# Performance work log

Hardware: AMD Instinct MI355X
Metric: run time of the kernel (lower is better)

## Reference

```python
import jax, jax.numpy as jnp
import numpy as np

B = 131072
E = 116            # embedding dim; 12 + E = 128 = layer_sizes[0]
H = 256            # MLP hidden
LATENT = 64

PAIRS = [(0, 1), (0, 2), (1, 2)]
IDS = np.array([[0, 3, 4], [1, 5, 6], [2, 7, 8]])  # ids_in_config, indexed by pair count


def setup_inputs() -> dict:
    key = jax.random.key(0)
    ks = jax.random.split(key, 12)
    d_in = 12 + E  # 128
    s = lambda k, shape, fan_in: jax.random.normal(k, shape, jnp.float32) / np.sqrt(fan_in)
    return {
        "initial_s": jax.random.normal(ks[0], (B, 9), jnp.float32),
        "current_s": jax.random.normal(ks[1], (B, 9), jnp.float32),
        "embeddings": jax.random.normal(ks[2], (B, E), jnp.float32),
        "W1": s(ks[3], (d_in, H), d_in),
        "b1": jnp.zeros((H,), jnp.float32),
        "W2": s(ks[4], (H, H), H),
        "b2": jnp.zeros((H,), jnp.float32),
        "Wm": s(ks[5], (H, LATENT), H),
        "bm": jnp.zeros((LATENT,), jnp.float32),
        "Wv": s(ks[6], (H, LATENT), H),
        "bv": jnp.zeros((LATENT,), jnp.float32),
    }


def _build_inp(initial_s, current_s, embeddings):
    # Replicates the pairwise one-hot + gather + concat construction.
    bsz = initial_s.shape[0]
    eye = jnp.eye(3, dtype=initial_s.dtype)
    feats = []
    for c, (i, j) in enumerate(PAIRS):
        oh = jnp.broadcast_to(jnp.concatenate([eye[i], eye[j]]), (bsz, 6))
        idx = IDS[c]
        feats.append(jnp.concatenate(
            [oh, initial_s[:, idx], current_s[:, idx], embeddings], axis=-1))
    return jnp.stack(feats)  # (3, B, 12+E)


def reference(initial_s, current_s, embeddings, W1, b1, W2, b2, Wm, bm, Wv, bv):
    inp = _build_inp(initial_s, current_s, embeddings)      # (3, B, 128)
    x = jax.nn.relu(jnp.einsum('pbi,ih->pbh', inp, W1) + b1)  # (3, B, 256)
    x = jax.nn.relu(jnp.einsum('pbh,hk->pbk', x, W2) + b2)    # (3, B, 256)
    means = jnp.einsum('pbh,hl->pbl', x, Wm) + bm             # (3, B, 64)
    log_vars = jnp.einsum('pbh,hl->pbl', x, Wv) + bv          # (3, B, 64)
    return (means, log_vars)
```

## Files before the change

kernel.cpp:

```cpp
#include <hip/hip_runtime.h>

typedef __attribute__((ext_vector_type(8))) __bf16 bf16x8;
typedef __attribute__((ext_vector_type(4))) float f32x4;
typedef unsigned int u32;
typedef unsigned long long u64;
typedef unsigned short u16;

#define NB 131072
#define TPB 8

__device__ __forceinline__ u16 f2bf(float f) {
  unsigned int u = __builtin_bit_cast(unsigned int, f);
  u += 0x7fffu + ((u >> 16) & 1u);
  return (u16)(u >> 16);
}

#define INP_ADDR(r, byte) (((r) << 8) + ((byte) ^ (((r) & 7) << 4)))
#define X_ADDR(r, byte)   (((r) << 9) + ((byte) ^ (((r) & 7) << 4)))

__global__ void prep_kernel(const float* __restrict__ W1, const float* __restrict__ b1,
                            const float* __restrict__ W2,
                            const float* __restrict__ Wm, const float* __restrict__ Wv,
                            u16* __restrict__ W1f, u16* __restrict__ W2f,
                            u16* __restrict__ Whf, float* __restrict__ b1p) {
  int tid = blockIdx.x * 256 + threadIdx.x;
  int NT = gridDim.x * 256;
  for (int i = tid; i < 32768; i += NT) {
    int j = i & 7, lane = (i >> 3) & 63, f = i >> 9;
    int nf = f & 15, kf = f >> 4;
    int n = nf * 16 + (lane & 15);
    int k = kf * 32 + 8 * (lane >> 4) + j;
    W1f[i] = f2bf(W1[k * 256 + n]);
  }
  for (int i = tid; i < 65536; i += NT) {
    int j = i & 7, lane = (i >> 3) & 63, f = i >> 9;
    int nf = f & 15, kf = f >> 4;
    int n = nf * 16 + (lane & 15);
    int k = kf * 32 + 8 * (lane >> 4) + j;
    W2f[i] = f2bf(W2[k * 256 + n]);
  }
  for (int i = tid; i < 32768; i += NT) {
    int j = i & 7, lane = (i >> 3) & 63, f = i >> 9;
    int nf = f & 7, kf = f >> 3;
    int n = nf * 16 + (lane & 15);
    int k = kf * 32 + 8 * (lane >> 4) + j;
    Whf[i] = f2bf(n < 64 ? Wm[k * 64 + n] : Wv[k * 64 + (n - 64)]);
  }
  if (tid < 768) {
    int p = tid >> 8, h = tid & 255;
    const int r1[3] = {0, 0, 1};
    const int r2[3] = {4, 5, 5};
    b1p[tid] = b1[h] + W1[r1[p] * 256 + h] + W1[r2[p] * 256 + h];
  }
}

__global__ __launch_bounds__(512, 2) void fused_kernel(
    const float* __restrict__ init_s, const float* __restrict__ cur_s,
    const float* __restrict__ emb,
    const u16* __restrict__ W1f, const u16* __restrict__ W2f,
    const u16* __restrict__ Whf,
    const float* __restrict__ b1p, const float* __restrict__ b2,
    const float* __restrict__ bm, const float* __restrict__ bv,
    float* __restrict__ out) {
  extern __shared__ char smem[];
  char* inp = smem;
  char* x1  = smem + 16384;
  char* x2  = smem + 49152;
  char* ost = x1;
  float* sbI = (float*)(smem + 81920);
  float* sbC = (float*)(smem + 81920 + 2304);

  const int t = threadIdx.x;
  const int lane = t & 63;
  const int wave = t >> 6;
  const int ql = lane & 15, qw = lane >> 4;

  bf16x8 w1r[4][2];
#pragma unroll
  for (int kf = 0; kf < 4; ++kf)
#pragma unroll
    for (int ni = 0; ni < 2; ++ni)
      w1r[kf][ni] = *(const bf16x8*)(W1f + (size_t)((kf * 16 + wave * 2 + ni) * 64 + lane) * 8);
  bf16x8 w2r[8][2];
#pragma unroll
  for (int kf = 0; kf < 8; ++kf)
#pragma unroll
    for (int ni = 0; ni < 2; ++ni)
      w2r[kf][ni] = *(const bf16x8*)(W2f + (size_t)((kf * 16 + wave * 2 + ni) * 64 + lane) * 8);
  bf16x8 whr[8];
#pragma unroll
  for (int kf = 0; kf < 8; ++kf)
    whr[kf] = *(const bf16x8*)(Whf + (size_t)((kf * 8 + wave) * 64 + lane) * 8);

  const int hn = wave * 16 + qw * 4;
  const f32x4 hbv = (hn < 64) ? *(const f32x4*)(bm + hn) : *(const f32x4*)(bv + hn - 64);

  if (t < 64) {
    *(u64*)(inp + INP_ADDR(t, 0)) = 0ull;
    *(u32*)(inp + INP_ADDR(t, 8)) = 0u;
  }

  const int IDSa[3] = {0, 1, 2};
  const int IDSb[3] = {3, 5, 7};
  const int IDSc[3] = {4, 6, 8};

#pragma unroll 1
  for (int it = 0; it < TPB; ++it) {
    const int b0 = (blockIdx.x * TPB + it) * 64;

    for (int i = t; i < 64 * 29; i += 512) {
      int r = i / 29;
      int c4 = i - r * 29;
      const float4 v = *(const float4*)(emb + (size_t)(b0 + r) * 116 + c4 * 4);
      u64 pk = (u64)f2bf(v.x) | ((u64)f2bf(v.y) << 16)
             | ((u64)f2bf(v.z) << 32) | ((u64)f2bf(v.w) << 48);
      *(u64*)(inp + INP_ADDR(r, 24 + 8 * c4)) = pk;
    }
    if (t < 288) {
      int which = t >= 144;
      int idx = which ? t - 144 : t;
      const float* src = which ? cur_s : init_s;
      float* dst = which ? sbC : sbI;
      ((float4*)dst)[idx] = ((const float4*)(src + (size_t)b0 * 9))[idx];
    }

#pragma unroll 1
    for (int p = 0; p < 3; ++p) {
      if (p == 0) __syncthreads();
      if (t < 64) {
        float a0 = sbI[t * 9 + IDSa[p]], a1 = sbI[t * 9 + IDSb[p]], a2 = sbI[t * 9 + IDSc[p]];
        float c0 = sbC[t * 9 + IDSa[p]], c1 = sbC[t * 9 + IDSb[p]], c2 = sbC[t * 9 + IDSc[p]];
        *(u32*)(inp + INP_ADDR(t, 12)) = (u32)f2bf(a0) | ((u32)f2bf(a1) << 16);
        *(u32*)(inp + INP_ADDR(t, 16)) = (u32)f2bf(a2) | ((u32)f2bf(c0) << 16);
        *(u32*)(inp + INP_ADDR(t, 20)) = (u32)f2bf(c1) | ((u32)f2bf(c2) << 16);
      }
      __syncthreads();

      {
        f32x4 acc[4][2];
#pragma unroll
        for (int ni = 0; ni < 2; ++ni) {
          f32x4 bb = *(const f32x4*)(b1p + p * 256 + wave * 32 + ni * 16 + qw * 4);
#pragma unroll
          for (int bf = 0; bf < 4; ++bf) acc[bf][ni] = bb;
        }
#pragma unroll
        for (int kf = 0; kf < 4; ++kf) {
          bf16x8 b[4];
#pragma unroll
          for (int bf = 0; bf < 4; ++bf)
            b[bf] = *(const bf16x8*)(inp + INP_ADDR(bf * 16 + ql, kf * 64 + qw * 16));
#pragma unroll
          for (int ni = 0; ni < 2; ++ni)
#pragma unroll
            for (int bf = 0; bf < 4; ++bf)
              acc[bf][ni] = __builtin_amdgcn_mfma_f32_16x16x32_bf16(w1r[kf][ni], b[bf], acc[bf][ni], 0, 0, 0);
        }
#pragma unroll
        for (int bf = 0; bf < 4; ++bf)
#pragma unroll
          for (int ni = 0; ni < 2; ++ni) {
            int row = bf * 16 + ql;
            int byte = wave * 64 + ni * 32 + qw * 8;
            f32x4 v = acc[bf][ni];
            float v0 = v[0] > 0.f ? v[0] : 0.f, v1 = v[1] > 0.f ? v[1] : 0.f;
            float v2 = v[2] > 0.f ? v[2] : 0.f, v3 = v[3] > 0.f ? v[3] : 0.f;
            u64 pk = (u64)f2bf(v0) | ((u64)f2bf(v1) << 16)
                   | ((u64)f2bf(v2) << 32) | ((u64)f2bf(v3) << 48);
            *(u64*)(x1 + X_ADDR(row, byte)) = pk;
          }
      }
      __syncthreads();

      {
        f32x4 acc[4][2];
#pragma unroll
        for (int ni = 0; ni < 2; ++ni) {
          f32x4 bb = *(const f32x4*)(b2 + wave * 32 + ni * 16 + qw * 4);
#pragma unroll
          for (int bf = 0; bf < 4; ++bf) acc[bf][ni] = bb;
        }
#pragma unroll
        for (int kf = 0; kf < 8; ++kf) {
          bf16x8 b[4];
#pragma unroll
          for (int bf = 0; bf < 4; ++bf)
            b[bf] = *(const bf16x8*)(x1 + X_ADDR(bf * 16 + ql, kf * 64 + qw * 16));
#pragma unroll
          for (int ni = 0; ni < 2; ++ni)
#pragma unroll
            for (int bf = 0; bf < 4; ++bf)
              acc[bf][ni] = __builtin_amdgcn_mfma_f32_16x16x32_bf16(w2r[kf][ni], b[bf], acc[bf][ni], 0, 0, 0);
        }
#pragma unroll
        for (int bf = 0; bf < 4; ++bf)
#pragma unroll
          for (int ni = 0; ni < 2; ++ni) {
            int row = bf * 16 + ql;
            int byte = wave * 64 + ni * 32 + qw * 8;
            f32x4 v = acc[bf][ni];
            float v0 = v[0] > 0.f ? v[0] : 0.f, v1 = v[1] > 0.f ? v[1] : 0.f;
            float v2 = v[2] > 0.f ? v[2] : 0.f, v3 = v[3] > 0.f ? v[3] : 0.f;
            u64 pk = (u64)f2bf(v0) | ((u64)f2bf(v1) << 16)
                   | ((u64)f2bf(v2) << 32) | ((u64)f2bf(v3) << 48);
            *(u64*)(x2 + X_ADDR(row, byte)) = pk;
          }
      }
      __syncthreads();

      {
        f32x4 hacc[4];
#pragma unroll
        for (int bf = 0; bf < 4; ++bf) hacc[bf] = hbv;
#pragma unroll
        for (int kf = 0; kf < 8; ++kf) {
          bf16x8 b[4];
#pragma unroll
          for (int bf = 0; bf < 4; ++bf)
            b[bf] = *(const bf16x8*)(x2 + X_ADDR(bf * 16 + ql, kf * 64 + qw * 16));
#pragma unroll
          for (int bf = 0; bf < 4; ++bf)
            hacc[bf] = __builtin_amdgcn_mfma_f32_16x16x32_bf16(whr[kf], b[bf], hacc[bf], 0, 0, 0);
        }
#pragma unroll
        for (int bf = 0; bf < 4; ++bf) {
          int row = bf * 16 + ql;
          int byte = wave * 64 + qw * 16;
          *(f32x4*)(ost + row * 512 + (byte ^ ((row & 7) << 4))) = hacc[bf];
        }
      }
      __syncthreads();

      for (int i = t; i < 64 * 32; i += 512) {
        int r = i >> 5, c4 = i & 31;
        float4 v = *(const float4*)(ost + r * 512 + ((c4 * 16) ^ ((r & 7) << 4)));
        size_t off;
        if (c4 < 16)
          off = ((size_t)p * NB + b0 + r) * 64 + (size_t)c4 * 4;
        else
          off = (size_t)3 * NB * 64 + ((size_t)p * NB + b0 + r) * 64 + (size_t)(c4 - 16) * 4;
        *(float4*)(out + off) = v;
      }
    }
  }
}

extern "C" void kernel_launch(void* const* d_in, const int* in_sizes, int n_in,
                              void* d_out, int out_size, void* d_ws, size_t ws_size,
                              hipStream_t stream) {
  (void)in_sizes; (void)n_in; (void)out_size; (void)ws_size;
  const float* init_s = (const float*)d_in[0];
  const float* cur_s  = (const float*)d_in[1];
  const float* emb    = (const float*)d_in[2];
  const float* W1 = (const float*)d_in[3];
  const float* b1 = (const float*)d_in[4];
  const float* W2 = (const float*)d_in[5];
  const float* b2 = (const float*)d_in[6];
  const float* Wm = (const float*)d_in[7];
  const float* bm = (const float*)d_in[8];
  const float* Wv = (const float*)d_in[9];
  const float* bv = (const float*)d_in[10];

  u16* W1f = (u16*)d_ws;
  u16* W2f = (u16*)((char*)d_ws + 65536);
  u16* Whf = (u16*)((char*)d_ws + 196608);
  float* b1p = (float*)((char*)d_ws + 262144);

  prep_kernel<<<128, 256, 0, stream>>>(W1, b1, W2, Wm, Wv, W1f, W2f, Whf, b1p);

  const int lds_bytes = 16384 + 32768 + 32768 + 4608;
  (void)hipFuncSetAttribute((const void*)fused_kernel,
                            hipFuncAttributeMaxDynamicSharedMemorySize, lds_bytes);
  fused_kernel<<<NB / (64 * TPB), 512, lds_bytes, stream>>>(init_s, cur_s, emb, W1f, W2f, Whf,
                                                            b1p, b2, bm, bv, (float*)d_out);
}
```

Baseline: 149.8 us.

## Stream weights from cache, raise occupancy, write outputs directly, prefetch next tile

Weight fragments are no longer held in registers for the whole kernel. They are reloaded from global/L2 inside each k-loop, and launch bounds go from 2 to 4 blocks per SM with TPB halved to 4. The pair and tile loops are flattened into one step loop. The next tile's inputs are loaded during the head-GEMM stage, removing one barrier. Outputs are written straight from MFMA registers instead of being staged through LDS, the LDS staging for the state vectors is dropped, and hardware v_cvt_pk_bf16_f32 packs replace the manual bf16 rounding. The risks are extra repeated weight-load traffic and less coalesced 16-byte output stores, and the 82 KB LDS per block may not actually allow 4 blocks per SM.

New measurement: 232.4 us. +55.1%, slower.

```diff
diff --git a/kernel.cpp b/kernel.cpp
--- a/kernel.cpp
+++ b/kernel.cpp
@@ -7,12 +7,18 @@
 typedef unsigned short u16;
 
 #define NB 131072
-#define TPB 8
+#define TPB 4
 
 __device__ __forceinline__ u16 f2bf(float f) {
   unsigned int u = __builtin_bit_cast(unsigned int, f);
   u += 0x7fffu + ((u >> 16) & 1u);
   return (u16)(u >> 16);
+}
+
+__device__ __forceinline__ u32 cvt_pk(float lo, float hi) {
+  u32 r;
+  asm("v_cvt_pk_bf16_f32 %0, %1, %2" : "=v"(r) : "v"(lo), "v"(hi));
+  return r;
 }
 
 #define INP_ADDR(r, byte) (((r) << 8) + ((byte) ^ (((r) & 7) << 4)))
@@ -54,7 +60,7 @@
   }
 }
 
-__global__ __launch_bounds__(512, 2) void fused_kernel(
+__global__ __launch_bounds__(512, 4) void fused_kernel(
     const float* __restrict__ init_s, const float* __restrict__ cur_s,
     const float* __restrict__ emb,
     const u16* __restrict__ W1f, const u16* __restrict__ W2f,
@@ -66,182 +72,157 @@
   char* inp = smem;
   char* x1  = smem + 16384;
   char* x2  = smem + 49152;
-  char* ost = x1;
-  float* sbI = (float*)(smem + 81920);
-  float* sbC = (float*)(smem + 81920 + 2304);
 
   const int t = threadIdx.x;
   const int lane = t & 63;
   const int wave = t >> 6;
   const int ql = lane & 15, qw = lane >> 4;
 
-  bf16x8 w1r[4][2];
-#pragma unroll
-  for (int kf = 0; kf < 4; ++kf)
-#pragma unroll
-    for (int ni = 0; ni < 2; ++ni)
-      w1r[kf][ni] = *(const bf16x8*)(W1f + (size_t)((kf * 16 + wave * 2 + ni) * 64 + lane) * 8);
-  bf16x8 w2r[8][2];
-#pragma unroll
-  for (int kf = 0; kf < 8; ++kf)
-#pragma unroll
-    for (int ni = 0; ni < 2; ++ni)
-      w2r[kf][ni] = *(const bf16x8*)(W2f + (size_t)((kf * 16 + wave * 2 + ni) * 64 + lane) * 8);
-  bf16x8 whr[8];
-#pragma unroll
-  for (int kf = 0; kf < 8; ++kf)
-    whr[kf] = *(const bf16x8*)(Whf + (size_t)((kf * 8 + wave) * 64 + lane) * 8);
-
   const int hn = wave * 16 + qw * 4;
-  const f32x4 hbv = (hn < 64) ? *(const f32x4*)(bm + hn) : *(const f32x4*)(bv + hn - 64);
+  const f32x4 hb = (hn < 64) ? *(const f32x4*)(bm + hn) : *(const f32x4*)(bv + hn - 64);
+  float* const hout = (hn < 64) ? (out + hn) : (out + (size_t)3 * NB * 64 + (hn - 64));
+
+  const int IA[3] = {0, 1, 2};
+  const int IB[3] = {3, 5, 7};
+  const int IC[3] = {4, 6, 8};
 
   if (t < 64) {
     *(u64*)(inp + INP_ADDR(t, 0)) = 0ull;
     *(u32*)(inp + INP_ADDR(t, 8)) = 0u;
   }
-
-  const int IDSa[3] = {0, 1, 2};
-  const int IDSb[3] = {3, 5, 7};
-  const int IDSc[3] = {4, 6, 8};
+  {
+    const size_t nb0 = (size_t)blockIdx.x * TPB * 64;
+    for (int i = t; i < 64 * 29; i += 512) {
+      int r = i / 29, c4 = i - r * 29;
+      const float4 v = *(const float4*)(emb + (nb0 + r) * 116 + c4 * 4);
+      u64 pk = (u64)cvt_pk(v.x, v.y) | ((u64)cvt_pk(v.z, v.w) << 32);
+      *(u64*)(inp + INP_ADDR(r, 24 + 8 * c4)) = pk;
+    }
+    if (t < 64) {
+      const float* isr = init_s + (nb0 + t) * 9;
+      const float* csr = cur_s + (nb0 + t) * 9;
+      *(u32*)(inp + INP_ADDR(t, 12)) = cvt_pk(isr[0], isr[3]);
+      *(u32*)(inp + INP_ADDR(t, 16)) = cvt_pk(isr[4], csr[0]);
+      *(u32*)(inp + INP_ADDR(t, 20)) = cvt_pk(csr[3], csr[4]);
+    }
+  }
+  __syncthreads();
 
 #pragma unroll 1
-  for (int it = 0; it < TPB; ++it) {
-    const int b0 = (blockIdx.x * TPB + it) * 64;
-
-    for (int i = t; i < 64 * 29; i += 512) {
-      int r = i / 29;
-      int c4 = i - r * 29;
-      const float4 v = *(const float4*)(emb + (size_t)(b0 + r) * 116 + c4 * 4);
-      u64 pk = (u64)f2bf(v.x) | ((u64)f2bf(v.y) << 16)
-             | ((u64)f2bf(v.z) << 32) | ((u64)f2bf(v.w) << 48);
-      *(u64*)(inp + INP_ADDR(r, 24 + 8 * c4)) = pk;
-    }
-    if (t < 288) {
-      int which = t >= 144;
-      int idx = which ? t - 144 : t;
-      const float* src = which ? cur_s : init_s;
-      float* dst = which ? sbC : sbI;
-      ((float4*)dst)[idx] = ((const float4*)(src + (size_t)b0 * 9))[idx];
-    }
-
-#pragma unroll 1
-    for (int p = 0; p < 3; ++p) {
-      if (p == 0) __syncthreads();
-      if (t < 64) {
-        float a0 = sbI[t * 9 + IDSa[p]], a1 = sbI[t * 9 + IDSb[p]], a2 = sbI[t * 9 + IDSc[p]];
-        float c0 = sbC[t * 9 + IDSa[p]], c1 = sbC[t * 9 + IDSb[p]], c2 = sbC[t * 9 + IDSc[p]];
-        *(u32*)(inp + INP_ADDR(t, 12)) = (u32)f2bf(a0) | ((u32)f2bf(a1) << 16);
-        *(u32*)(inp + INP_ADDR(t, 16)) = (u32)f2bf(a2) | ((u32)f2bf(c0) << 16);
-        *(u32*)(inp + INP_ADDR(t, 20)) = (u32)f2bf(c1) | ((u32)f2bf(c2) << 16);
-      }
-      __syncthreads();
-
-      {
-        f32x4 acc[4][2];
+  for (int step = 0; step < 3 * TPB; ++step) {
+    const int p = step % 3;
+    const size_t b0 = (size_t)(blockIdx.x * TPB + step / 3) * 64;
+
+    {
+      f32x4 acc[4][2];
+#pragma unroll
+      for (int ni = 0; ni < 2; ++ni) {
+        f32x4 bb = *(const f32x4*)(b1p + p * 256 + wave * 32 + ni * 16 + qw * 4);
+#pragma unroll
+        for (int bf = 0; bf < 4; ++bf) acc[bf][ni] = bb;
+      }
+#pragma unroll
+      for (int kf = 0; kf < 4; ++kf) {
+        bf16x8 w0 = *(const bf16x8*)(W1f + (size_t)((kf * 16 + wave * 2 + 0) * 64 + lane) * 8);
+        bf16x8 w1 = *(const bf16x8*)(W1f + (size_t)((kf * 16 + wave * 2 + 1) * 64 + lane) * 8);
+        bf16x8 a[4];
+#pragma unroll
+        for (int bf = 0; bf < 4; ++bf)
+          a[bf] = *(const bf16x8*)(inp + INP_ADDR(bf * 16 + ql, kf * 64 + qw * 16));
+#pragma unroll
+        for (int bf = 0; bf < 4; ++bf)
+          acc[bf][0] = __builtin_amdgcn_mfma_f32_16x16x32_bf16(w0, a[bf], acc[bf][0], 0, 0, 0);
+#pragma unroll
+        for (int bf = 0; bf < 4; ++bf)
+          acc[bf][1] = __builtin_amdgcn_mfma_f32_16x16x32_bf16(w1, a[bf], acc[bf][1], 0, 0, 0);
+      }
+#pragma unroll
+      for (int bf = 0; bf < 4; ++bf)
 #pragma unroll
         for (int ni = 0; ni < 2; ++ni) {
-          f32x4 bb = *(const f32x4*)(b1p + p * 256 + wave * 32 + ni * 16 + qw * 4);
-#pragma unroll
-          for (int bf = 0; bf < 4; ++bf) acc[bf][ni] = bb;
-        }
-#pragma unroll
-        for (int kf = 0; kf < 4; ++kf) {
-          bf16x8 b[4];
-#pragma unroll
-          for (int bf = 0; bf < 4; ++bf)
-            b[bf] = *(const bf16x8*)(inp + INP_ADDR(bf * 16 + ql, kf * 64 + qw * 16));
-#pragma unroll
-          for (int ni = 0; ni < 2; ++ni)
-#pragma unroll
-            for (int bf = 0; bf < 4; ++bf)
-              acc[bf][ni] = __builtin_amdgcn_mfma_f32_16x16x32_bf16(w1r[kf][ni], b[bf], acc[bf][ni], 0, 0, 0);
-        }
-#pragma unroll
-        for (int bf = 0; bf < 4; ++bf)
-#pragma unroll
-          for (int ni = 0; ni < 2; ++ni) {
-            int row = bf * 16 + ql;
-            int byte = wave * 64 + ni * 32 + qw * 8;
-            f32x4 v = acc[bf][ni];
-            float v0 = v[0] > 0.f ? v[0] : 0.f, v1 = v[1] > 0.f ? v[1] : 0.f;
-            float v2 = v[2] > 0.f ? v[2] : 0.f, v3 = v[3] > 0.f ? v[3] : 0.f;
-            u64 pk = (u64)f2bf(v0) | ((u64)f2bf(v1) << 16)
-                   | ((u64)f2bf(v2) << 32) | ((u64)f2bf(v3) << 48);
-            *(u64*)(x1 + X_ADDR(row, byte)) = pk;
+          f32x4 v = acc[bf][ni];
+          u64 pk = (u64)cvt_pk(fmaxf(v[0], 0.f), fmaxf(v[1], 0.f))
+                 | ((u64)cvt_pk(fmaxf(v[2], 0.f), fmaxf(v[3], 0.f)) << 32);
+          *(u64*)(x1 + X_ADDR(bf * 16 + ql, wave * 64 + ni * 32 + qw * 8)) = pk;
+        }
+    }
+    __syncthreads();
+
+    {
+      f32x4 acc[4][2];
+#pragma unroll
+      for (int ni = 0; ni < 2; ++ni) {
+        f32x4 bb = *(const f32x4*)(b2 + wave * 32 + ni * 16 + qw * 4);
+#pragma unroll
+        for (int bf = 0; bf < 4; ++bf) acc[bf][ni] = bb;
+      }
+#pragma unroll 4
+      for (int kf = 0; kf < 8; ++kf) {
+        bf16x8 w0 = *(const bf16x8*)(W2f + (size_t)((kf * 16 + wave * 2 + 0) * 64 + lane) * 8);
+        bf16x8 w1 = *(const bf16x8*)(W2f + (size_t)((kf * 16 + wave * 2 + 1) * 64 + lane) * 8);
+        bf16x8 a[4];
+#pragma unroll
+        for (int bf = 0; bf < 4; ++bf)
+          a[bf] = *(const bf16x8*)(x1 + X_ADDR(bf * 16 + ql, kf * 64 + qw * 16));
+#pragma unroll
+        for (int bf = 0; bf < 4; ++bf)
+          acc[bf][0] = __builtin_amdgcn_mfma_f32_16x16x32_bf16(w0, a[bf], acc[bf][0], 0, 0, 0);
+#pragma unroll
+        for (int bf = 0; bf < 4; ++bf)
+          acc[bf][1] = __builtin_amdgcn_mfma_f32_16x16x32_bf16(w1, a[bf], acc[bf][1], 0, 0, 0);
+      }
+#pragma unroll
+      for (int bf = 0; bf < 4; ++bf)
+#pragma unroll
+        for (int ni = 0; ni < 2; ++ni) {
+          f32x4 v = acc[bf][ni];
+          u64 pk = (u64)cvt_pk(fmaxf(v[0], 0.f), fmaxf(v[1], 0.f))
+                 | ((u64)cvt_pk(fmaxf(v[2], 0.f), fmaxf(v[3], 0.f)) << 32);
+          *(u64*)(x2 + X_ADDR(bf * 16 + ql, wave * 64 + ni * 32 + qw * 8)) = pk;
+        }
+    }
+    __syncthreads();
+
+    {
+      f32x4 hacc[4];
+#pragma unroll
+      for (int bf = 0; bf < 4; ++bf) hacc[bf] = hb;
+#pragma unroll
+      for (int kf = 0; kf < 8; ++kf) {
+        bf16x8 w = *(const bf16x8*)(Whf + (size_t)((kf * 8 + wave) * 64 + lane) * 8);
+        bf16x8 a[4];
+#pragma unroll
+        for (int bf = 0; bf < 4; ++bf)
+          a[bf] = *(const bf16x8*)(x2 + X_ADDR(bf * 16 + ql, kf * 64 + qw * 16));
+#pragma unroll
+        for (int bf = 0; bf < 4; ++bf)
+          hacc[bf] = __builtin_amdgcn_mfma_f32_16x16x32_bf16(w, a[bf], hacc[bf], 0, 0, 0);
+      }
+#pragma unroll
+      for (int bf = 0; bf < 4; ++bf)
+        *(f32x4*)(hout + ((size_t)p * NB + b0 + bf * 16 + ql) * 64) = hacc[bf];
+
+      if (step + 1 < 3 * TPB) {
+        const int np = (step + 1) % 3;
+        const size_t nb0 = (size_t)(blockIdx.x * TPB + (step + 1) / 3) * 64;
+        if (np == 0) {
+          for (int i = t; i < 64 * 29; i += 512) {
+            int r = i / 29, c4 = i - r * 29;
+            const float4 v = *(const float4*)(emb + (nb0 + r) * 116 + c4 * 4);
+            u64 pk = (u64)cvt_pk(v.x, v.y) | ((u64)cvt_pk(v.z, v.w) << 32);
+            *(u64*)(inp + INP_ADDR(r, 24 + 8 * c4)) = pk;
           }
-      }
-      __syncthreads();
-
-      {
-        f32x4 acc[4][2];
-#pragma unroll
-        for (int ni = 0; ni < 2; ++ni) {
-          f32x4 bb = *(const f32x4*)(b2 + wave * 32 + ni * 16 + qw * 4);
-#pragma unroll
-          for (int bf = 0; bf < 4; ++bf) acc[bf][ni] = bb;
-        }
-#pragma unroll
-        for (int kf = 0; kf < 8; ++kf) {
-          bf16x8 b[4];
-#pragma unroll
-          for (int bf = 0; bf < 4; ++bf)
-            b[bf] = *(const bf16x8*)(x1 + X_ADDR(bf * 16 + ql, kf * 64 + qw * 16));
-#pragma unroll
-          for (int ni = 0; ni < 2; ++ni)
-#pragma unroll
-            for (int bf = 0; bf < 4; ++bf)
-              acc[bf][ni] = __builtin_amdgcn_mfma_f32_16x16x32_bf16(w2r[kf][ni], b[bf], acc[bf][ni], 0, 0, 0);
-        }
-#pragma unroll
-        for (int bf = 0; bf < 4; ++bf)
-#pragma unroll
-          for (int ni = 0; ni < 2; ++ni) {
-            int row = bf * 16 + ql;
-            int byte = wave * 64 + ni * 32 + qw * 8;
-            f32x4 v = acc[bf][ni];
-            float v0 = v[0] > 0.f ? v[0] : 0.f, v1 = v[1] > 0.f ? v[1] : 0.f;
-            float v2 = v[2] > 0.f ? v[2] : 0.f, v3 = v[3] > 0.f ? v[3] : 0.f;
-            u64 pk = (u64)f2bf(v0) | ((u64)f2bf(v1) << 16)
-                   | ((u64)f2bf(v2) << 32) | ((u64)f2bf(v3) << 48);
-            *(u64*)(x2 + X_ADDR(row, byte)) = pk;
-          }
-      }
-      __syncthreads();
-
-      {
-        f32x4 hacc[4];
-#pragma unroll
-        for (int bf = 0; bf < 4; ++bf) hacc[bf] = hbv;
-#pragma unroll
-        for (int kf = 0; kf < 8; ++kf) {
-          bf16x8 b[4];
-#pragma unroll
-          for (int bf = 0; bf < 4; ++bf)
-            b[bf] = *(const bf16x8*)(x2 + X_ADDR(bf * 16 + ql, kf * 64 + qw * 16));
-#pragma unroll
-          for (int bf = 0; bf < 4; ++bf)
-            hacc[bf] = __builtin_amdgcn_mfma_f32_16x16x32_bf16(whr[kf], b[bf], hacc[bf], 0, 0, 0);
-        }
-#pragma unroll
-        for (int bf = 0; bf < 4; ++bf) {
-          int row = bf * 16 + ql;
-          int byte = wave * 64 + qw * 16;
-          *(f32x4*)(ost + row * 512 + (byte ^ ((row & 7) << 4))) = hacc[bf];
-        }
-      }
-      __syncthreads();
-
-      for (int i = t; i < 64 * 32; i += 512) {
-        int r = i >> 5, c4 = i & 31;
-        float4 v = *(const float4*)(ost + r * 512 + ((c4 * 16) ^ ((r & 7) << 4)));
-        size_t off;
-        if (c4 < 16)
-          off = ((size_t)p * NB + b0 + r) * 64 + (size_t)c4 * 4;
-        else
-          off = (size_t)3 * NB * 64 + ((size_t)p * NB + b0 + r) * 64 + (size_t)(c4 - 16) * 4;
-        *(float4*)(out + off) = v;
-      }
-    }
+        }
+        if (t < 64) {
+          const float* isr = init_s + (nb0 + t) * 9;
+          const float* csr = cur_s + (nb0 + t) * 9;
+          *(u32*)(inp + INP_ADDR(t, 12)) = cvt_pk(isr[IA[np]], isr[IB[np]]);
+          *(u32*)(inp + INP_ADDR(t, 16)) = cvt_pk(isr[IC[np]], csr[IA[np]]);
+          *(u32*)(inp + INP_ADDR(t, 20)) = cvt_pk(csr[IB[np]], csr[IC[np]]);
+        }
+      }
+    }
+    __syncthreads();
   }
 }
 
@@ -268,7 +249,7 @@
 
   prep_kernel<<<128, 256, 0, stream>>>(W1, b1, W2, Wm, Wv, W1f, W2f, Whf, b1p);
 
-  const int lds_bytes = 16384 + 32768 + 32768 + 4608;
+  const int lds_bytes = 16384 + 32768 + 32768;
   (void)hipFuncSetAttribute((const void*)fused_kernel,
                             hipFuncAttributeMaxDynamicSharedMemorySize, lds_bytes);
   fused_kernel<<<NB / (64 * TPB), 512, lds_bytes, stream>>>(init_s, cur_s, emb, W1f, W2f, Whf,
```
